# Performance work log

Measured on AMD Instinct MI355X. Metric: run time of the kernel, lower is better.

The kernel has to match this reference:

```python
import jax, jax.numpy as jnp
import numpy as np
from jax import lax

B, S, H, NH, FF, L, V = 4, 512, 768, 12, 3072, 6, 30522
DH = H // NH


def layer_norm(x, g, b, eps=1e-12):
    mu = x.mean(-1, keepdims=True)
    var = ((x - mu) ** 2).mean(-1, keepdims=True)
    return (x - mu) * lax.rsqrt(var + eps) * g + b


def crf_log_likelihood(emissions, tags, mask, start_t, end_t, trans):
    # torchcrf math, batch_first: emissions [B,S,T], tags [B,S], mask [B,S] bool
    Bn = emissions.shape[0]
    maskf = mask.astype(emissions.dtype)
    barange = jnp.arange(Bn)
    # gold-path (numerator) score
    first = tags[:, 0]
    num = start_t[first] + emissions[barange, 0, first]
    prev, cur = tags[:, :-1], tags[:, 1:]
    trans_sc = trans[prev, cur]                                   # [B,S-1]
    em_sc = jnp.take_along_axis(emissions[:, 1:], cur[..., None], axis=2)[..., 0]
    num = num + jnp.sum((trans_sc + em_sc) * maskf[:, 1:], axis=1)
    last_idx = jnp.sum(mask, axis=1).astype(jnp.int32) - 1
    num = num + end_t[tags[barange, last_idx]]
    # partition function via forward-algorithm scan over time
    alpha0 = start_t[None, :] + emissions[:, 0]                   # [B,T]
    def step(alpha, xs):
        em_t, m_t = xs
        nxt = jax.nn.logsumexp(alpha[:, :, None] + trans[None] + em_t[:, None, :], axis=1)
        return jnp.where(m_t[:, None], nxt, alpha), None
    xs = (jnp.swapaxes(emissions[:, 1:], 0, 1), jnp.swapaxes(mask[:, 1:], 0, 1))
    alpha, _ = lax.scan(step, alpha0, xs)
    logZ = jax.nn.logsumexp(alpha + end_t[None, :], axis=1)
    return num - logZ


def bert_qa_emissions(input_ids, attention_mask, token_type_ids, word_emb, pos_emb, type_emb,
                      emb_ln_g, emb_ln_b, Wq, bq, Wk, bk, Wv, bv, Wo, bo, ln1_g, ln1_b,
                      W1, b1, W2, b2, ln2_g, ln2_b, qa_w, qa_b):
    x = word_emb[input_ids] + pos_emb[None, :S] + type_emb[token_type_ids]
    x = layer_norm(x, emb_ln_g, emb_ln_b)
    bias = (1.0 - attention_mask.astype(jnp.float32))[:, None, None, :] * -1e9
    scale = 1.0 / float(np.sqrt(DH))
    for l in range(L):
        q = (x @ Wq[l] + bq[l]).reshape(B, S, NH, DH)
        k = (x @ Wk[l] + bk[l]).reshape(B, S, NH, DH)
        v = (x @ Wv[l] + bv[l]).reshape(B, S, NH, DH)
        att = jnp.einsum('bqhd,bkhd->bhqk', q, k) * scale + bias
        p = jax.nn.softmax(att, axis=-1)
        o = jnp.einsum('bhqk,bkhd->bqhd', p, v).reshape(B, S, H)
        x = layer_norm(x + o @ Wo[l] + bo[l], ln1_g[l], ln1_b[l])
        h = jax.nn.gelu(x @ W1[l] + b1[l], approximate=False)
        x = layer_norm(x + h @ W2[l] + b2[l], ln2_g[l], ln2_b[l])
    # qa_outputs: start_logits = col 0, end_logits = col 1 == stack([start,end], dim=2)
    return x @ qa_w + qa_b                                        # [B,S,2]


def setup_inputs() -> dict:
    key = jax.random.key(0)
    ks = jax.random.split(key, 20)
    g = lambda k, shape: jax.random.normal(k, shape, jnp.float32) * 0.02
    u = lambda k, shape: jax.random.uniform(k, shape, jnp.float32, -0.1, 0.1)
    return {
        'input_ids': jax.random.randint(ks[0], (B, S), 0, V),
        'attention_mask': jnp.ones((B, S), jnp.int32),
        'token_type_ids': jnp.zeros((B, S), jnp.int32),
        'start_positions': jax.random.randint(ks[1], (B,), 0, 200),
        'end_positions': jax.random.randint(ks[2], (B,), 0, 400),
        'word_emb': g(ks[3], (V, H)),
        'pos_emb': g(ks[4], (S, H)),
        'type_emb': g(ks[5], (2, H)),
        'emb_ln_g': jnp.ones((H,), jnp.float32), 'emb_ln_b': jnp.zeros((H,), jnp.float32),
        'Wq': g(ks[6], (L, H, H)), 'bq': jnp.zeros((L, H), jnp.float32),
        'Wk': g(ks[7], (L, H, H)), 'bk': jnp.zeros((L, H), jnp.float32),
        'Wv': g(ks[8], (L, H, H)), 'bv': jnp.zeros((L, H), jnp.float32),
        'Wo': g(ks[9], (L, H, H)), 'bo': jnp.zeros((L, H), jnp.float32),
        'ln1_g': jnp.ones((L, H), jnp.float32), 'ln1_b': jnp.zeros((L, H), jnp.float32),
        'W1': g(ks[10], (L, H, FF)), 'b1': jnp.zeros((L, FF), jnp.float32),
        'W2': g(ks[11], (L, FF, H)), 'b2': jnp.zeros((L, H), jnp.float32),
        'ln2_g': jnp.ones((L, H), jnp.float32), 'ln2_b': jnp.zeros((L, H), jnp.float32),
        'qa_w': g(ks[12], (H, 2)), 'qa_b': jnp.zeros((2,), jnp.float32),
        'crf_start': u(ks[13], (2,)), 'crf_end': u(ks[14], (2,)), 'crf_trans': u(ks[15], (2, 2)),
    }


def reference(input_ids, attention_mask, token_type_ids, start_positions, end_positions,
              word_emb, pos_emb, type_emb, emb_ln_g, emb_ln_b, Wq, bq, Wk, bk, Wv, bv,
              Wo, bo, ln1_g, ln1_b, W1, b1, W2, b2, ln2_g, ln2_b, qa_w, qa_b,
              crf_start, crf_end, crf_trans):
    emissions = bert_qa_emissions(input_ids, attention_mask, token_type_ids, word_emb, pos_emb,
                                  type_emb, emb_ln_g, emb_ln_b, Wq, bq, Wk, bk, Wv, bv, Wo, bo,
                                  ln1_g, ln1_b, W1, b1, W2, b2, ln2_g, ln2_b, qa_w, qa_b)
    # labels[i, start:end+1] = 1 when 0 <= start <= end < S, else all zeros (matches torch loop)
    pos = jnp.arange(S)
    sp = start_positions[:, None]
    ep = end_positions[:, None]
    valid = (sp >= 0) & (sp < S) & (ep >= 0) & (ep < S) & (sp <= ep)
    labels = jnp.where(valid & (pos >= sp) & (pos <= ep), 1, 0)
    mask = attention_mask.astype(bool)
    llh = crf_log_likelihood(emissions, labels, mask, crf_start, crf_end, crf_trans)
    return -jnp.sum(llh)  # torchcrf reduction='sum'; loss = -crf(...)
```

## Files before the change

### kernel.cpp

```cpp
#include <hip/hip_runtime.h>
#include <hip/hip_bf16.h>
#include <math.h>

#define B_  4
#define S_  512
#define H_  768
#define NH_ 12
#define DH_ 64
#define FF_ 3072
#define L_  6
#define V_  30522
#define QKVN 2304
#define M_  (B_ * S_)

typedef short s16x8 __attribute__((ext_vector_type(8)));
typedef short s16x4v __attribute__((ext_vector_type(4)));
typedef float f32x4 __attribute__((ext_vector_type(4)));

__device__ __forceinline__ void gload_lds16(const void* g, void* l) {
    __builtin_amdgcn_global_load_lds(
        (const __attribute__((address_space(1))) void*)g,
        (__attribute__((address_space(3))) void*)l,
        16, 0, 0);
}

__device__ __forceinline__ ushort f2bu(float x) {
    __hip_bfloat16 h = __float2bfloat16(x);
    return *(ushort*)&h;
}

__device__ __forceinline__ s16x8 lds_frag(const ushort* p) {
    s16x4v lo = *(const s16x4v*)p;
    s16x4v hi = *(const s16x4v*)(p + 4);
    return __builtin_shufflevector(lo, hi, 0, 1, 2, 3, 4, 5, 6, 7);
}

__device__ __forceinline__ s16x8 lds_frag16(const ushort* p) {
    return *(const s16x8*)p;
}

__device__ __forceinline__ void embed_body(
    const int* __restrict__ ids, const int* __restrict__ tt,
    const float* __restrict__ wemb, const float* __restrict__ pemb,
    const float* __restrict__ temb, const float* __restrict__ g,
    const float* __restrict__ bb, float* __restrict__ x,
    __hip_bfloat16* __restrict__ xb, float* red)
{
    const int t = blockIdx.x;
    const int s = t % S_;
    const int tid = threadIdx.x;

    const float* wr = wemb + (size_t)ids[t] * H_;
    const float* pr = pemb + (size_t)s * H_;
    const float* tr = temb + (size_t)tt[t] * H_;

    float v[3];
    float sum = 0.f;
#pragma unroll
    for (int i = 0; i < 3; i++) {
        int c = tid + i * 256;
        v[i] = wr[c] + pr[c] + tr[c];
        sum += v[i];
    }
    red[tid] = sum; __syncthreads();
    for (int st = 128; st > 0; st >>= 1) { if (tid < st) red[tid] += red[tid + st]; __syncthreads(); }
    const float mean = red[0] / (float)H_;
    __syncthreads();
    float s2 = 0.f;
#pragma unroll
    for (int i = 0; i < 3; i++) { float d = v[i] - mean; s2 += d * d; }
    red[tid] = s2; __syncthreads();
    for (int st = 128; st > 0; st >>= 1) { if (tid < st) red[tid] += red[tid + st]; __syncthreads(); }
    const float rstd = rsqrtf(red[0] / (float)H_ + 1e-12f);
#pragma unroll
    for (int i = 0; i < 3; i++) {
        int c = tid + i * 256;
        float o = (v[i] - mean) * rstd * g[c] + bb[c];
        x[(size_t)t * H_ + c] = o;
        xb[(size_t)t * H_ + c] = __float2bfloat16(o);
    }
}

__global__ __launch_bounds__(256) void prep_embed_kernel(
    const float* __restrict__ Wq, const float* __restrict__ Wk,
    const float* __restrict__ Wv, const float* __restrict__ Wo,
    const float* __restrict__ W1, const float* __restrict__ W2,
    const float* __restrict__ bq, const float* __restrict__ bk,
    const float* __restrict__ bv,
    ushort* __restrict__ Wt_qkv, ushort* __restrict__ Wt_o,
    ushort* __restrict__ Wt_1, ushort* __restrict__ Wt_2,
    float* __restrict__ b_qkv,
    const int* __restrict__ ids, const int* __restrict__ tt,
    const float* __restrict__ wemb, const float* __restrict__ pemb,
    const float* __restrict__ temb, const float* __restrict__ eg,
    const float* __restrict__ eb, float* __restrict__ x,
    __hip_bfloat16* __restrict__ xb)
{
    __shared__ float tile[64][68];

    if (blockIdx.y == L_) {
        embed_body(ids, tt, wemb, pemb, temb, eg, eb, x, xb, (float*)tile);
        return;
    }

    const int l  = blockIdx.y;
    const int id = blockIdx.x;
    if (id >= 1737) return;
    const int tid = threadIdx.x;

    if (id >= 1728) {
        int i = (id - 1728) * 256 + tid;
        if (i < QKVN)
            b_qkv[(size_t)l * QKVN + i] =
                (i < H_) ? bq[l * H_ + i]
                         : ((i < 2 * H_) ? bk[l * H_ + i - H_] : bv[l * H_ + i - 2 * H_]);
        return;
    }

    const float* src; ushort* dst; int N, ncols, ktiles, t;
    if (id < 432) {
        const int mat = id / 144; t = id % 144;
        src = (mat == 0) ? (Wq + (size_t)l * H_ * H_)
            : (mat == 1) ? (Wk + (size_t)l * H_ * H_)
                         : (Wv + (size_t)l * H_ * H_);
        dst = Wt_qkv + (size_t)l * 3 * H_ * H_ + (size_t)mat * H_ * H_;
        N = H_; ncols = 12; ktiles = 12;
    } else if (id < 576) {
        t = id - 432;
        src = Wo + (size_t)l * H_ * H_;
        dst = Wt_o + (size_t)l * H_ * H_;
        N = H_; ncols = 12; ktiles = 12;
    } else if (id < 1152) {
        t = id - 576;
        src = W1 + (size_t)l * H_ * FF_;
        dst = Wt_1 + (size_t)l * H_ * FF_;
        N = FF_; ncols = 48; ktiles = 12;
    } else {
        t = id - 1152;
        src = W2 + (size_t)l * FF_ * H_;
        dst = Wt_2 + (size_t)l * FF_ * H_;
        N = H_; ncols = 12; ktiles = 48;
    }

    const int n0 = (t % ncols) * 64;
    const int k0 = (t / ncols) * 64;

    const int lr = tid >> 4;
    const int lc = tid & 15;
#pragma unroll
    for (int i = 0; i < 4; i++)
        *(f32x4*)&tile[lr + 16 * i][lc * 4] =
            *(const f32x4*)&src[(size_t)(k0 + lr + 16 * i) * N + n0 + lc * 4];
    __syncthreads();

    const int rn = tid >> 2;
    const int kc = tid & 3;
    s16x8 o0, o1;
#pragma unroll
    for (int j = 0; j < 8; j++) o0[j] = (short)f2bu(tile[kc * 16 + j][rn]);
#pragma unroll
    for (int j = 0; j < 8; j++) o1[j] = (short)f2bu(tile[kc * 16 + 8 + j][rn]);
    ushort* dp = dst + ((size_t)(n0 >> 6) * ktiles + (k0 >> 6)) * 4096 + tid * 16;
    *(s16x8*)dp       = o0;
    *(s16x8*)(dp + 8) = o1;
}

#define TM 128
#define TN 128
#define TK 64

template<int EPI, int OUTBF, int NS>
__global__ __launch_bounds__(256) void gemm_mfma_kernel(
    const ushort* __restrict__ A, const ushort* __restrict__ Bt,
    const float* __restrict__ bias, void* __restrict__ Cout,
    int M, int K, int N)
{
    __shared__ alignas(16) ushort As[2][TM * TK];
    __shared__ alignas(16) ushort Bs[2][TN * TK];
    const int tid  = threadIdx.x;
    const int lane = tid & 63;
    const int wave = tid >> 6;
    const int m0 = blockIdx.y * TM;
    const int n0 = blockIdx.x * TN;
    const int wm = (wave >> 1) * 64;
    const int wn = (wave & 1) * 64;

    const int Ksub = K / NS;
    const int Kt   = K >> 6;
    int kt0 = 0;
    if (NS > 1) {
        A  += (size_t)blockIdx.z * Ksub;
        kt0 = blockIdx.z * (Ksub >> 6);
    }

    f32x4 acc[4][4];
#pragma unroll
    for (int i = 0; i < 4; i++)
#pragma unroll
        for (int j = 0; j < 4; j++)
            acc[i][j] = (f32x4){0.f, 0.f, 0.f, 0.f};

    const int r8 = lane >> 3;
    const int sl = lane & 7;
    const int gk = (sl ^ r8) * 8;
    const ushort* aSrc[4];
    const ushort* bSrc[4];
    int dOff[4];
#pragma unroll
    for (int c = 0; c < 4; c++) {
        const int R = wave * 32 + c * 8;
        aSrc[c] = A + (size_t)(m0 + R + r8) * K + gk;
        const int n = n0 + R + r8;
        bSrc[c] = Bt + ((size_t)(n >> 6) * Kt + kt0) * 4096 + (n & 63) * 64 + gk;
        dOff[c] = R * TK;
    }

    const int fr = lane & 15;
    const int q4 = lane >> 4;
    int offA[4][2], offB[4][2];
#pragma unroll
    for (int i = 0; i < 4; i++) {
        const int rowA = wm + i * 16 + fr;
        const int rowB = wn + i * 16 + fr;
#pragma unroll
        for (int ks = 0; ks < 2; ks++) {
            offA[i][ks] = rowA * TK + (((ks * 4 + q4) ^ (rowA & 7)) * 8);
            offB[i][ks] = rowB * TK + (((ks * 4 + q4) ^ (rowB & 7)) * 8);
        }
    }

    const int niter = Ksub / TK;

#pragma unroll
    for (int c = 0; c < 4; c++) {
        gload_lds16(aSrc[c], &As[0][dOff[c]]);
        gload_lds16(bSrc[c], &Bs[0][dOff[c]]);
    }

    int cur = 0;
    for (int it = 0; it < niter; ++it) {
        __syncthreads();
        if (it + 1 < niter) {
            const int koff = (it + 1) * TK;
            const size_t boff = (size_t)(it + 1) * 4096;
#pragma unroll
            for (int c = 0; c < 4; c++) {
                gload_lds16(aSrc[c] + koff, &As[cur ^ 1][dOff[c]]);
                gload_lds16(bSrc[c] + boff, &Bs[cur ^ 1][dOff[c]]);
            }
        }

#pragma unroll
        for (int ks = 0; ks < 2; ks++) {
            s16x8 af[4], bf[4];
#pragma unroll
            for (int i = 0; i < 4; i++) af[i] = lds_frag16(&As[cur][offA[i][ks]]);
#pragma unroll
            for (int j = 0; j < 4; j++) bf[j] = lds_frag16(&Bs[cur][offB[j][ks]]);
#pragma unroll
            for (int i = 0; i < 4; i++)
#pragma unroll
                for (int j = 0; j < 4; j++)
                    acc[i][j] = __builtin_amdgcn_mfma_f32_16x16x32_bf16(
                        af[i], bf[j], acc[i][j], 0, 0, 0);
        }
        cur ^= 1;
    }

    const int ecol = lane & 15;
    const int erow = (lane >> 4) * 4;
    float* outF = (float*)Cout + (size_t)blockIdx.z * M * N;
#pragma unroll
    for (int j = 0; j < 4; j++) {
        const int gcol = n0 + wn + j * 16 + ecol;
        const float bv = (NS == 1 || blockIdx.z == 0) ? bias[gcol] : 0.f;
#pragma unroll
        for (int i = 0; i < 4; i++) {
#pragma unroll
            for (int r = 0; r < 4; r++) {
                const int grow = m0 + wm + i * 16 + erow + r;
                float v = acc[i][j][r] + bv;
                if (EPI == 1) v = v * 0.5f * (1.0f + erff(v * 0.70710678118654752f));
                if (OUTBF)
                    ((ushort*)Cout)[(size_t)grow * N + gcol] = f2bu(v);
                else
                    outF[(size_t)grow * N + gcol] = v;
            }
        }
    }
}

#define VST 68

__global__ __launch_bounds__(256) void flash_attn_mfma_kernel(
    const ushort* __restrict__ QKV, const int* __restrict__ amask,
    __hip_bfloat16* __restrict__ Octx)
{
    const int q0 = blockIdx.x * 64, h = blockIdx.y, b = blockIdx.z;
    const int tid = threadIdx.x, lane = tid & 63, wave = tid >> 6;
    __shared__ ushort Qs[64 * VST];
    __shared__ ushort Ks[64 * VST];
    __shared__ ushort Vt[64 * VST];
    __shared__ ushort Ps[4][16 * VST];
    __shared__ float biasS[S_];

    for (int i = tid; i < S_; i += 256)
        biasS[i] = amask[b * S_ + i] ? 0.f : -1e9f;

    {
        const ushort* qb = QKV + (size_t)(b * S_ + q0) * QKVN + h * DH_;
        const int q = tid >> 2, dg = (tid & 3) * 16;
        s16x8 v0 = *(const s16x8*)(qb + (size_t)q * QKVN + dg);
        s16x8 v1 = *(const s16x8*)(qb + (size_t)q * QKVN + dg + 8);
        ushort* d = &Qs[q * VST + dg];
        *(s16x4v*)(d)      = __builtin_shufflevector(v0, v0, 0, 1, 2, 3);
        *(s16x4v*)(d + 4)  = __builtin_shufflevector(v0, v0, 4, 5, 6, 7);
        *(s16x4v*)(d + 8)  = __builtin_shufflevector(v1, v1, 0, 1, 2, 3);
        *(s16x4v*)(d + 12) = __builtin_shufflevector(v1, v1, 4, 5, 6, 7);
    }
    __syncthreads();

    const int fm = lane & 15;
    const int fk = (lane >> 4) * 8;

    const s16x8 aq0 = lds_frag(&Qs[(wave * 16 + fm) * VST + fk]);
    const s16x8 aq1 = lds_frag(&Qs[(wave * 16 + fm) * VST + 32 + fk]);

    f32x4 acc[4];
#pragma unroll
    for (int j = 0; j < 4; j++) acc[j] = (f32x4){0.f, 0.f, 0.f, 0.f};
    float m_i[4], l_i[4];
#pragma unroll
    for (int r = 0; r < 4; r++) { m_i[r] = -INFINITY; l_i[r] = 0.f; }

    for (int kt = 0; kt < S_; kt += 64) {
        __syncthreads();
        {
            const ushort* kb = QKV + (size_t)(b * S_ + kt) * QKVN + H_ + h * DH_;
            const int ky = tid >> 2, dg = (tid & 3) * 16;
            s16x8 v0 = *(const s16x8*)(kb + (size_t)ky * QKVN + dg);
            s16x8 v1 = *(const s16x8*)(kb + (size_t)ky * QKVN + dg + 8);
            ushort* d = &Ks[ky * VST + dg];
            *(s16x4v*)(d)      = __builtin_shufflevector(v0, v0, 0, 1, 2, 3);
            *(s16x4v*)(d + 4)  = __builtin_shufflevector(v0, v0, 4, 5, 6, 7);
            *(s16x4v*)(d + 8)  = __builtin_shufflevector(v1, v1, 0, 1, 2, 3);
            *(s16x4v*)(d + 12) = __builtin_shufflevector(v1, v1, 4, 5, 6, 7);
        }
        {
            const ushort* vb = QKV + (size_t)(b * S_ + kt) * QKVN + 2 * H_ + h * DH_;
            const int d = tid & 63, kg = tid >> 6;
#pragma unroll
            for (int kp = 0; kp < 8; kp++) {
                const int key = kg * 16 + kp * 2;
                ushort u0 = vb[(size_t)key * QKVN + d];
                ushort u1 = vb[(size_t)(key + 1) * QKVN + d];
                ushort2 u; u.x = u0; u.y = u1;
                *(ushort2*)&Vt[d * VST + key] = u;
            }
        }
        __syncthreads();

        f32x4 sc[4];
#pragma unroll
        for (int jj = 0; jj < 4; jj++) {
            s16x8 b0 = lds_frag(&Ks[(jj * 16 + fm) * VST + fk]);
            s16x8 b1 = lds_frag(&Ks[(jj * 16 + fm) * VST + 32 + fk]);
            f32x4 z = (f32x4){0.f, 0.f, 0.f, 0.f};
            z = __builtin_amdgcn_mfma_f32_16x16x32_bf16(aq0, b0, z, 0, 0, 0);
            z = __builtin_amdgcn_mfma_f32_16x16x32_bf16(aq1, b1, z, 0, 0, 0);
            sc[jj] = z;
        }

#pragma unroll
        for (int r = 0; r < 4; r++) {
            float mx = -INFINITY;
#pragma unroll
            for (int jj = 0; jj < 4; jj++) {
                float v = sc[jj][r] * 0.125f + biasS[kt + jj * 16 + fm];
                sc[jj][r] = v;
                mx = fmaxf(mx, v);
            }
#pragma unroll
            for (int msk = 1; msk < 16; msk <<= 1) mx = fmaxf(mx, __shfl_xor(mx, msk));
            const float newm = fmaxf(m_i[r], mx);
            const float alpha = __expf(m_i[r] - newm);
            m_i[r] = newm;
            float rs = 0.f;
#pragma unroll
            for (int jj = 0; jj < 4; jj++) {
                float p = __expf(sc[jj][r] - newm);
                sc[jj][r] = p; rs += p;
            }
#pragma unroll
            for (int msk = 1; msk < 16; msk <<= 1) rs += __shfl_xor(rs, msk);
            l_i[r] = l_i[r] * alpha + rs;
#pragma unroll
            for (int jj = 0; jj < 4; jj++) acc[jj][r] *= alpha;
        }

#pragma unroll
        for (int jj = 0; jj < 4; jj++)
#pragma unroll
            for (int r = 0; r < 4; r++)
                Ps[wave][((lane >> 4) * 4 + r) * VST + jj * 16 + fm] = f2bu(sc[jj][r]);

        const s16x8 ap0 = lds_frag(&Ps[wave][fm * VST + fk]);
        const s16x8 ap1 = lds_frag(&Ps[wave][fm * VST + 32 + fk]);

#pragma unroll
        for (int jj = 0; jj < 4; jj++) {
            s16x8 b0 = lds_frag(&Vt[(jj * 16 + fm) * VST + fk]);
            s16x8 b1 = lds_frag(&Vt[(jj * 16 + fm) * VST + 32 + fk]);
            acc[jj] = __builtin_amdgcn_mfma_f32_16x16x32_bf16(ap0, b0, acc[jj], 0, 0, 0);
            acc[jj] = __builtin_amdgcn_mfma_f32_16x16x32_bf16(ap1, b1, acc[jj], 0, 0, 0);
        }
    }

#pragma unroll
    for (int r = 0; r < 4; r++) {
        const int q = q0 + wave * 16 + (lane >> 4) * 4 + r;
        const float inv = 1.0f / l_i[r];
        __hip_bfloat16* op = Octx + (size_t)(b * S_ + q) * H_ + h * DH_;
#pragma unroll
        for (int jj = 0; jj < 4; jj++)
            op[jj * 16 + fm] = __float2bfloat16(acc[jj][r] * inv);
    }
}

template<int NS, int QA>
__global__ __launch_bounds__(256) void add_ln_kernel(
    float* __restrict__ x, const float* __restrict__ delta,
    const float* __restrict__ g, const float* __restrict__ bb,
    __hip_bfloat16* __restrict__ xb,
    const float* __restrict__ qa_w, const float* __restrict__ qa_b,
    float* __restrict__ em)
{
    const int t = blockIdx.x;
    const int tid = threadIdx.x;
    __shared__ float red[256];
    __shared__ float red2[256];
    const size_t base = (size_t)t * H_;

    float v[3];
    float sum = 0.f;
#pragma unroll
    for (int i = 0; i < 3; i++) {
        int c = tid + i * 256;
        float d = x[base + c];
#pragma unroll
        for (int s = 0; s < NS; s++)
            d += delta[(size_t)s * M_ * H_ + base + c];
        v[i] = d;
        sum += d;
    }
    red[tid] = sum; __syncthreads();
    for (int st = 128; st > 0; st >>= 1) { if (tid < st) red[tid] += red[tid + st]; __syncthreads(); }
    const float mean = red[0] / (float)H_;
    __syncthreads();
    float s2 = 0.f;
#pragma unroll
    for (int i = 0; i < 3; i++) { float d = v[i] - mean; s2 += d * d; }
    red[tid] = s2; __syncthreads();
    for (int st = 128; st > 0; st >>= 1) { if (tid < st) red[tid] += red[tid + st]; __syncthreads(); }
    const float rstd = rsqrtf(red[0] / (float)H_ + 1e-12f);
    float s0 = 0.f, s1 = 0.f;
#pragma unroll
    for (int i = 0; i < 3; i++) {
        int c = tid + i * 256;
        float o = (v[i] - mean) * rstd * g[c] + bb[c];
        x[base + c] = o;
        xb[base + c] = __float2bfloat16(o);
        if (QA) {
            s0 += o * qa_w[c * 2 + 0];
            s1 += o * qa_w[c * 2 + 1];
        }
    }
    if (QA) {
        __syncthreads();
        red[tid] = s0; red2[tid] = s1; __syncthreads();
        for (int st = 128; st > 0; st >>= 1) {
            if (tid < st) { red[tid] += red[tid + st]; red2[tid] += red2[tid + st]; }
            __syncthreads();
        }
        if (tid == 0) {
            em[(size_t)t * 2 + 0] = red[0] + qa_b[0];
            em[(size_t)t * 2 + 1] = red2[0] + qa_b[1];
        }
    }
}

__device__ __forceinline__ float lse2(float a, float b) {
    float m = fmaxf(a, b);
    return m + log1pf(expf(-fabsf(a - b)));
}

__device__ __forceinline__ float4 lsem_comb(float4 a, float4 b) {
    float4 r;
    r.x = lse2(a.x + b.x, a.y + b.z);
    r.y = lse2(a.x + b.y, a.y + b.w);
    r.z = lse2(a.z + b.x, a.w + b.z);
    r.w = lse2(a.z + b.y, a.w + b.w);
    return r;
}

__global__ __launch_bounds__(256) void crf_parallel_kernel(
    const float* __restrict__ em, const int* __restrict__ amask,
    const int* __restrict__ spos, const int* __restrict__ epos,
    const float* __restrict__ startT, const float* __restrict__ endT,
    const float* __restrict__ trans, float* __restrict__ out)
{
    __shared__ float4 mats[B_][64];
    __shared__ float numred[B_][64];
    __shared__ float cntred[B_][64];
    __shared__ float llh[B_];
    const int tid = threadIdx.x;
    const int s = tid >> 6;
    const int j = tid & 63;
    const float NEG = -1e30f;

    const int sp = spos[s], ep = epos[s];
    const bool valid = (sp >= 0) && (sp < S_) && (ep >= 0) && (ep < S_) && (sp <= ep);
    const float* e = em + (size_t)s * S_ * 2;
    const int* mk = amask + s * S_;
    const float t00 = trans[0], t01 = trans[1], t10 = trans[2], t11 = trans[3];

    float4 C = make_float4(0.f, NEG, NEG, 0.f);
    float num = 0.f, cnt = 0.f;
#pragma unroll
    for (int k = 0; k < 8; k++) {
        const int t = j * 8 + 1 + k;
        float4 Mt = make_float4(0.f, NEG, NEG, 0.f);
        if (t < S_ && mk[t]) {
            const float e0 = e[2 * t], e1 = e[2 * t + 1];
            Mt = make_float4(t00 + e0, t01 + e1, t10 + e0, t11 + e1);
            const int tp = (valid && (t - 1) >= sp && (t - 1) <= ep) ? 1 : 0;
            const int tc = (valid && t >= sp && t <= ep) ? 1 : 0;
            const float tr = tp ? (tc ? t11 : t10) : (tc ? t01 : t00);
            num += tr + (tc ? e1 : e0);
            cnt += 1.f;
        }
        C = (k == 0) ? Mt : lsem_comb(C, Mt);
    }
    if (j == 0) {
        const int tag0 = (valid && 0 >= sp && 0 <= ep) ? 1 : 0;
        num += startT[tag0] + e[tag0];
        cnt += mk[0] ? 1.f : 0.f;
    }
    mats[s][j] = C;
    numred[s][j] = num;
    cntred[s][j] = cnt;
    __syncthreads();

    for (int st = 32; st >= 1; st >>= 1) {
        float4 a, b;
        const bool act = (j < st);
        if (act) { a = mats[s][2 * j]; b = mats[s][2 * j + 1]; }
        __syncthreads();
        if (act) mats[s][j] = lsem_comb(a, b);
        __syncthreads();
    }
    for (int st = 32; st >= 1; st >>= 1) {
        if (j < st) {
            numred[s][j] += numred[s][j + st];
            cntred[s][j] += cntred[s][j + st];
        }
        __syncthreads();
    }

    if (j == 0) {
        float numT = numred[s][0];
        const int last_idx = (int)(cntred[s][0] + 0.5f) - 1;
        const int ltag = (valid && last_idx >= sp && last_idx <= ep) ? 1 : 0;
        numT += endT[ltag];
        const float a00 = startT[0] + e[0];
        const float a01 = startT[1] + e[1];
        const float4 P = mats[s][0];
        const float aF0 = lse2(a00 + P.x, a01 + P.z);
        const float aF1 = lse2(a00 + P.y, a01 + P.w);
        const float logZ = lse2(aF0 + endT[0], aF1 + endT[1]);
        llh[s] = numT - logZ;
    }
    __syncthreads();
    if (tid == 0)
        out[0] = -(llh[0] + llh[1] + llh[2] + llh[3]);
}

extern "C" void kernel_launch(void* const* d_in, const int* in_sizes, int n_in,
                              void* d_out, int out_size, void* d_ws, size_t ws_size,
                              hipStream_t stream)
{
    const int*   input_ids  = (const int*)  d_in[0];
    const int*   attn_mask  = (const int*)  d_in[1];
    const int*   token_type = (const int*)  d_in[2];
    const int*   start_pos  = (const int*)  d_in[3];
    const int*   end_pos    = (const int*)  d_in[4];
    const float* word_emb   = (const float*)d_in[5];
    const float* pos_emb    = (const float*)d_in[6];
    const float* type_emb   = (const float*)d_in[7];
    const float* emb_ln_g   = (const float*)d_in[8];
    const float* emb_ln_b   = (const float*)d_in[9];
    const float* Wq         = (const float*)d_in[10];
    const float* bq         = (const float*)d_in[11];
    const float* Wk         = (const float*)d_in[12];
    const float* bk         = (const float*)d_in[13];
    const float* Wv         = (const float*)d_in[14];
    const float* bv         = (const float*)d_in[15];
    const float* Wo         = (const float*)d_in[16];
    const float* bo         = (const float*)d_in[17];
    const float* ln1_g      = (const float*)d_in[18];
    const float* ln1_b      = (const float*)d_in[19];
    const float* W1         = (const float*)d_in[20];
    const float* b1         = (const float*)d_in[21];
    const float* W2         = (const float*)d_in[22];
    const float* b2         = (const float*)d_in[23];
    const float* ln2_g      = (const float*)d_in[24];
    const float* ln2_b      = (const float*)d_in[25];
    const float* qa_w       = (const float*)d_in[26];
    const float* qa_b       = (const float*)d_in[27];
    const float* crf_start  = (const float*)d_in[28];
    const float* crf_end    = (const float*)d_in[29];
    const float* crf_trans  = (const float*)d_in[30];
    float* out = (float*)d_out;

    float*  x      = (float*)d_ws;
    float*  tmp768 = x + (size_t)M_ * H_;
    float*  emis   = tmp768 + (size_t)4 * M_ * H_;
    float*  b_qkv  = emis + (size_t)M_ * 2;
    ushort* xb     = (ushort*)(b_qkv + (size_t)L_ * QKVN);
    ushort* qkvb   = xb + (size_t)M_ * H_;
    ushort* ctxb   = qkvb + (size_t)M_ * QKVN;
    ushort* hb     = ctxb + (size_t)M_ * H_;
    ushort* Wt_qkv = hb + (size_t)M_ * FF_;
    ushort* Wt_o   = Wt_qkv + (size_t)L_ * QKVN * H_;
    ushort* Wt_1   = Wt_o + (size_t)L_ * H_ * H_;
    ushort* Wt_2   = Wt_1 + (size_t)L_ * H_ * FF_;

    dim3 blk(256);

    prep_embed_kernel<<<dim3(2048, L_ + 1), blk, 0, stream>>>(
        Wq, Wk, Wv, Wo, W1, W2, bq, bk, bv,
        Wt_qkv, Wt_o, Wt_1, Wt_2, b_qkv,
        input_ids, token_type, word_emb, pos_emb, type_emb,
        emb_ln_g, emb_ln_b, x, (__hip_bfloat16*)xb);

    const dim3 gQKV(QKVN / TN, M_ / TM);
    const dim3 gO(H_ / TN, M_ / TM, 2);
    const dim3 gF1(FF_ / TN, M_ / TM);
    const dim3 gF2(H_ / TN, M_ / TM, 4);
    const dim3 gA(S_ / 64, NH_, B_);

    for (int l = 0; l < L_; l++) {
        gemm_mfma_kernel<0, 1, 1><<<gQKV, blk, 0, stream>>>(
            xb, Wt_qkv + (size_t)l * QKVN * H_, b_qkv + (size_t)l * QKVN,
            qkvb, M_, H_, QKVN);

        flash_attn_mfma_kernel<<<gA, blk, 0, stream>>>(
            qkvb, attn_mask, (__hip_bfloat16*)ctxb);

        gemm_mfma_kernel<0, 0, 2><<<gO, blk, 0, stream>>>(
            ctxb, Wt_o + (size_t)l * H_ * H_, bo + l * H_, tmp768, M_, H_, H_);
        add_ln_kernel<2, 0><<<M_, blk, 0, stream>>>(
            x, tmp768, ln1_g + l * H_, ln1_b + l * H_,
            (__hip_bfloat16*)xb, nullptr, nullptr, nullptr);

        gemm_mfma_kernel<1, 1, 1><<<gF1, blk, 0, stream>>>(
            xb, Wt_1 + (size_t)l * H_ * FF_, b1 + l * FF_, hb, M_, H_, FF_);
        gemm_mfma_kernel<0, 0, 4><<<gF2, blk, 0, stream>>>(
            hb, Wt_2 + (size_t)l * FF_ * H_, b2 + l * H_, tmp768, M_, FF_, H_);
        if (l == L_ - 1)
            add_ln_kernel<4, 1><<<M_, blk, 0, stream>>>(
                x, tmp768, ln2_g + l * H_, ln2_b + l * H_,
                (__hip_bfloat16*)xb, qa_w, qa_b, emis);
        else
            add_ln_kernel<4, 0><<<M_, blk, 0, stream>>>(
                x, tmp768, ln2_g + l * H_, ln2_b + l * H_,
                (__hip_bfloat16*)xb, nullptr, nullptr, nullptr);
    }

    crf_parallel_kernel<<<1, 256, 0, stream>>>(emis, attn_mask, start_pos, end_pos,
                                               crf_start, crf_end, crf_trans, out);
}
```

Before: 1.013 ms.

## Overlap next-layer weight conversion with current layer's QKV, attention and FFN1 kernels

The upfront prep kernel now converts only layer 0 weights, alongside the embedding. Conversion of layer l+1's QKV, Wo/W1 and W2 tiles is spread across extra blocks appended to the QKV GEMM, attention and FFN1 launches of layer l. This hides fp32-to-bf16 transpose work in the tails and idle slots of compute kernels, shrinking the large serial prep launch. In exchange it adds grid padding, extra kernel parameters and shared-memory aliasing, and the extra blocks compete for bandwidth with the main work.

```diff
diff --git a/kernel.cpp b/kernel.cpp
--- a/kernel.cpp
+++ b/kernel.cpp
@@ -39,49 +39,8 @@
     return *(const s16x8*)p;
 }
 
-__device__ __forceinline__ void embed_body(
-    const int* __restrict__ ids, const int* __restrict__ tt,
-    const float* __restrict__ wemb, const float* __restrict__ pemb,
-    const float* __restrict__ temb, const float* __restrict__ g,
-    const float* __restrict__ bb, float* __restrict__ x,
-    __hip_bfloat16* __restrict__ xb, float* red)
-{
-    const int t = blockIdx.x;
-    const int s = t % S_;
-    const int tid = threadIdx.x;
-
-    const float* wr = wemb + (size_t)ids[t] * H_;
-    const float* pr = pemb + (size_t)s * H_;
-    const float* tr = temb + (size_t)tt[t] * H_;
-
-    float v[3];
-    float sum = 0.f;
-#pragma unroll
-    for (int i = 0; i < 3; i++) {
-        int c = tid + i * 256;
-        v[i] = wr[c] + pr[c] + tr[c];
-        sum += v[i];
-    }
-    red[tid] = sum; __syncthreads();
-    for (int st = 128; st > 0; st >>= 1) { if (tid < st) red[tid] += red[tid + st]; __syncthreads(); }
-    const float mean = red[0] / (float)H_;
-    __syncthreads();
-    float s2 = 0.f;
-#pragma unroll
-    for (int i = 0; i < 3; i++) { float d = v[i] - mean; s2 += d * d; }
-    red[tid] = s2; __syncthreads();
-    for (int st = 128; st > 0; st >>= 1) { if (tid < st) red[tid] += red[tid + st]; __syncthreads(); }
-    const float rstd = rsqrtf(red[0] / (float)H_ + 1e-12f);
-#pragma unroll
-    for (int i = 0; i < 3; i++) {
-        int c = tid + i * 256;
-        float o = (v[i] - mean) * rstd * g[c] + bb[c];
-        x[(size_t)t * H_ + c] = o;
-        xb[(size_t)t * H_ + c] = __float2bfloat16(o);
-    }
-}
-
-__global__ __launch_bounds__(256) void prep_embed_kernel(
+__device__ __forceinline__ void prep_tile_body(
+    int id, int l,
     const float* __restrict__ Wq, const float* __restrict__ Wk,
     const float* __restrict__ Wv, const float* __restrict__ Wo,
     const float* __restrict__ W1, const float* __restrict__ W2,
@@ -89,23 +48,8 @@
     const float* __restrict__ bv,
     ushort* __restrict__ Wt_qkv, ushort* __restrict__ Wt_o,
     ushort* __restrict__ Wt_1, ushort* __restrict__ Wt_2,
-    float* __restrict__ b_qkv,
-    const int* __restrict__ ids, const int* __restrict__ tt,
-    const float* __restrict__ wemb, const float* __restrict__ pemb,
-    const float* __restrict__ temb, const float* __restrict__ eg,
-    const float* __restrict__ eb, float* __restrict__ x,
-    __hip_bfloat16* __restrict__ xb)
-{
-    __shared__ float tile[64][68];
-
-    if (blockIdx.y == L_) {
-        embed_body(ids, tt, wemb, pemb, temb, eg, eb, x, xb, (float*)tile);
-        return;
-    }
-
-    const int l  = blockIdx.y;
-    const int id = blockIdx.x;
-    if (id >= 1737) return;
+    float* __restrict__ b_qkv, float (*tile)[68])
+{
     const int tid = threadIdx.x;
 
     if (id >= 1728) {
@@ -165,6 +109,98 @@
     *(s16x8*)(dp + 8) = o1;
 }
 
+__device__ __forceinline__ void prep_aux(
+    int mode, int t, int l,
+    const float* Wq, const float* Wk, const float* Wv, const float* Wo,
+    const float* W1, const float* W2,
+    const float* bq, const float* bk, const float* bv,
+    ushort* Wt_qkv, ushort* Wt_o, ushort* Wt_1, ushort* Wt_2,
+    float* b_qkv, float (*tile)[68])
+{
+    int canon;
+    if (mode == 0) {
+        if (t >= 441) return;
+        canon = (t < 432) ? t : 1728 + (t - 432);
+    } else if (mode == 1) {
+        if (t >= 720) return;
+        canon = 432 + t;
+    } else {
+        if (t >= 576) return;
+        canon = 1152 + t;
+    }
+    prep_tile_body(canon, l, Wq, Wk, Wv, Wo, W1, W2, bq, bk, bv,
+                   Wt_qkv, Wt_o, Wt_1, Wt_2, b_qkv, tile);
+}
+
+__device__ __forceinline__ void embed_body(
+    const int* __restrict__ ids, const int* __restrict__ tt,
+    const float* __restrict__ wemb, const float* __restrict__ pemb,
+    const float* __restrict__ temb, const float* __restrict__ g,
+    const float* __restrict__ bb, float* __restrict__ x,
+    __hip_bfloat16* __restrict__ xb, float* red)
+{
+    const int t = blockIdx.x;
+    const int s = t % S_;
+    const int tid = threadIdx.x;
+
+    const float* wr = wemb + (size_t)ids[t] * H_;
+    const float* pr = pemb + (size_t)s * H_;
+    const float* tr = temb + (size_t)tt[t] * H_;
+
+    float v[3];
+    float sum = 0.f;
+#pragma unroll
+    for (int i = 0; i < 3; i++) {
+        int c = tid + i * 256;
+        v[i] = wr[c] + pr[c] + tr[c];
+        sum += v[i];
+    }
+    red[tid] = sum; __syncthreads();
+    for (int st = 128; st > 0; st >>= 1) { if (tid < st) red[tid] += red[tid + st]; __syncthreads(); }
+    const float mean = red[0] / (float)H_;
+    __syncthreads();
+    float s2 = 0.f;
+#pragma unroll
+    for (int i = 0; i < 3; i++) { float d = v[i] - mean; s2 += d * d; }
+    red[tid] = s2; __syncthreads();
+    for (int st = 128; st > 0; st >>= 1) { if (tid < st) red[tid] += red[tid + st]; __syncthreads(); }
+    const float rstd = rsqrtf(red[0] / (float)H_ + 1e-12f);
+#pragma unroll
+    for (int i = 0; i < 3; i++) {
+        int c = tid + i * 256;
+        float o = (v[i] - mean) * rstd * g[c] + bb[c];
+        x[(size_t)t * H_ + c] = o;
+        xb[(size_t)t * H_ + c] = __float2bfloat16(o);
+    }
+}
+
+__global__ __launch_bounds__(256) void prep_embed_kernel(
+    const float* __restrict__ Wq, const float* __restrict__ Wk,
+    const float* __restrict__ Wv, const float* __restrict__ Wo,
+    const float* __restrict__ W1, const float* __restrict__ W2,
+    const float* __restrict__ bq, const float* __restrict__ bk,
+    const float* __restrict__ bv,
+    ushort* __restrict__ Wt_qkv, ushort* __restrict__ Wt_o,
+    ushort* __restrict__ Wt_1, ushort* __restrict__ Wt_2,
+    float* __restrict__ b_qkv,
+    const int* __restrict__ ids, const int* __restrict__ tt,
+    const float* __restrict__ wemb, const float* __restrict__ pemb,
+    const float* __restrict__ temb, const float* __restrict__ eg,
+    const float* __restrict__ eb, float* __restrict__ x,
+    __hip_bfloat16* __restrict__ xb)
+{
+    __shared__ __align__(16) float tile[64][68];
+
+    if (blockIdx.y == 1) {
+        embed_body(ids, tt, wemb, pemb, temb, eg, eb, x, xb, (float*)tile);
+        return;
+    }
+    const int id = blockIdx.x;
+    if (id < 1737)
+        prep_tile_body(id, 0, Wq, Wk, Wv, Wo, W1, W2, bq, bk, bv,
+                       Wt_qkv, Wt_o, Wt_1, Wt_2, b_qkv, tile);
+}
+
 #define TM 128
 #define TN 128
 #define TK 64
@@ -173,10 +209,27 @@
 __global__ __launch_bounds__(256) void gemm_mfma_kernel(
     const ushort* __restrict__ A, const ushort* __restrict__ Bt,
     const float* __restrict__ bias, void* __restrict__ Cout,
-    int M, int K, int N)
+    int M, int K, int N,
+    int auxMode, int lnext,
+    const float* Wq, const float* Wk, const float* Wv, const float* Wo,
+    const float* W1, const float* W2,
+    const float* bq, const float* bk, const float* bv,
+    ushort* Wt_qkv, ushort* Wt_o, ushort* Wt_1, ushort* Wt_2,
+    float* b_qkv)
 {
     __shared__ alignas(16) ushort As[2][TM * TK];
     __shared__ alignas(16) ushort Bs[2][TN * TK];
+
+    const int NX = N / TN;
+    if ((int)blockIdx.x >= NX) {
+        if (auxMode >= 0 && blockIdx.z == 0) {
+            const int t = ((int)blockIdx.x - NX) * gridDim.y + blockIdx.y;
+            prep_aux(auxMode, t, lnext, Wq, Wk, Wv, Wo, W1, W2, bq, bk, bv,
+                     Wt_qkv, Wt_o, Wt_1, Wt_2, b_qkv, (float(*)[68])As);
+        }
+        return;
+    }
+
     const int tid  = threadIdx.x;
     const int lane = tid & 63;
     const int wave = tid >> 6;
@@ -294,15 +347,33 @@
 
 __global__ __launch_bounds__(256) void flash_attn_mfma_kernel(
     const ushort* __restrict__ QKV, const int* __restrict__ amask,
-    __hip_bfloat16* __restrict__ Octx)
-{
+    __hip_bfloat16* __restrict__ Octx,
+    int auxMode, int lnext,
+    const float* Wq, const float* Wk, const float* Wv, const float* Wo,
+    const float* W1, const float* W2,
+    const float* bq, const float* bk, const float* bv,
+    ushort* Wt_qkv, ushort* Wt_o, ushort* Wt_1, ushort* Wt_2,
+    float* b_qkv)
+{
+    __shared__ __align__(16) char smem[36864];
+    ushort* const Qs  = (ushort*)smem;
+    ushort* const Ks  = (ushort*)(smem + 8704);
+    ushort* const Vt  = (ushort*)(smem + 17408);
+    ushort* const Ps  = (ushort*)(smem + 26112);
+    float*  const biasS = (float*)(smem + 34816);
+
+    if ((int)blockIdx.x >= S_ / 64) {
+        if (auxMode >= 0) {
+            const int t = ((int)blockIdx.x - S_ / 64) * 48
+                        + (int)blockIdx.y * 4 + (int)blockIdx.z;
+            prep_aux(auxMode, t, lnext, Wq, Wk, Wv, Wo, W1, W2, bq, bk, bv,
+                     Wt_qkv, Wt_o, Wt_1, Wt_2, b_qkv, (float(*)[68])smem);
+        }
+        return;
+    }
+
     const int q0 = blockIdx.x * 64, h = blockIdx.y, b = blockIdx.z;
     const int tid = threadIdx.x, lane = tid & 63, wave = tid >> 6;
-    __shared__ ushort Qs[64 * VST];
-    __shared__ ushort Ks[64 * VST];
-    __shared__ ushort Vt[64 * VST];
-    __shared__ ushort Ps[4][16 * VST];
-    __shared__ float biasS[S_];
 
     for (int i = tid; i < S_; i += 256)
         biasS[i] = amask[b * S_ + i] ? 0.f : -1e9f;
@@ -398,14 +469,15 @@
             for (int jj = 0; jj < 4; jj++) acc[jj][r] *= alpha;
         }
 
+        ushort* const Pw = Ps + wave * 16 * VST;
 #pragma unroll
         for (int jj = 0; jj < 4; jj++)
 #pragma unroll
             for (int r = 0; r < 4; r++)
-                Ps[wave][((lane >> 4) * 4 + r) * VST + jj * 16 + fm] = f2bu(sc[jj][r]);
-
-        const s16x8 ap0 = lds_frag(&Ps[wave][fm * VST + fk]);
-        const s16x8 ap1 = lds_frag(&Ps[wave][fm * VST + 32 + fk]);
+                Pw[((lane >> 4) * 4 + r) * VST + jj * 16 + fm] = f2bu(sc[jj][r]);
+
+        const s16x8 ap0 = lds_frag(&Pw[fm * VST + fk]);
+        const s16x8 ap1 = lds_frag(&Pw[fm * VST + 32 + fk]);
 
 #pragma unroll
         for (int jj = 0; jj < 4; jj++) {
@@ -637,36 +709,53 @@
 
     dim3 blk(256);
 
-    prep_embed_kernel<<<dim3(2048, L_ + 1), blk, 0, stream>>>(
+    prep_embed_kernel<<<dim3(2048, 2), blk, 0, stream>>>(
         Wq, Wk, Wv, Wo, W1, W2, bq, bk, bv,
         Wt_qkv, Wt_o, Wt_1, Wt_2, b_qkv,
         input_ids, token_type, word_emb, pos_emb, type_emb,
         emb_ln_g, emb_ln_b, x, (__hip_bfloat16*)xb);
 
-    const dim3 gQKV(QKVN / TN, M_ / TM);
-    const dim3 gO(H_ / TN, M_ / TM, 2);
-    const dim3 gF1(FF_ / TN, M_ / TM);
-    const dim3 gF2(H_ / TN, M_ / TM, 4);
-    const dim3 gA(S_ / 64, NH_, B_);
-
     for (int l = 0; l < L_; l++) {
-        gemm_mfma_kernel<0, 1, 1><<<gQKV, blk, 0, stream>>>(
+        const bool host = (l + 1 < L_);
+        const int lnext = l + 1;
+
+        dim3 gQKVl(QKVN / TN + (host ? 28 : 0), M_ / TM);
+        gemm_mfma_kernel<0, 1, 1><<<gQKVl, blk, 0, stream>>>(
             xb, Wt_qkv + (size_t)l * QKVN * H_, b_qkv + (size_t)l * QKVN,
-            qkvb, M_, H_, QKVN);
-
-        flash_attn_mfma_kernel<<<gA, blk, 0, stream>>>(
-            qkvb, attn_mask, (__hip_bfloat16*)ctxb);
-
+            qkvb, M_, H_, QKVN,
+            host ? 0 : -1, lnext,
+            Wq, Wk, Wv, Wo, W1, W2, bq, bk, bv,
+            Wt_qkv, Wt_o, Wt_1, Wt_2, b_qkv);
+
+        dim3 gAl(S_ / 64 + (host ? 15 : 0), NH_, B_);
+        flash_attn_mfma_kernel<<<gAl, blk, 0, stream>>>(
+            qkvb, attn_mask, (__hip_bfloat16*)ctxb,
+            host ? 1 : -1, lnext,
+            Wq, Wk, Wv, Wo, W1, W2, bq, bk, bv,
+            Wt_qkv, Wt_o, Wt_1, Wt_2, b_qkv);
+
+        dim3 gO(H_ / TN, M_ / TM, 2);
         gemm_mfma_kernel<0, 0, 2><<<gO, blk, 0, stream>>>(
-            ctxb, Wt_o + (size_t)l * H_ * H_, bo + l * H_, tmp768, M_, H_, H_);
+            ctxb, Wt_o + (size_t)l * H_ * H_, bo + l * H_, tmp768, M_, H_, H_,
+            -1, 0, Wq, Wk, Wv, Wo, W1, W2, bq, bk, bv,
+            Wt_qkv, Wt_o, Wt_1, Wt_2, b_qkv);
         add_ln_kernel<2, 0><<<M_, blk, 0, stream>>>(
             x, tmp768, ln1_g + l * H_, ln1_b + l * H_,
             (__hip_bfloat16*)xb, nullptr, nullptr, nullptr);
 
-        gemm_mfma_kernel<1, 1, 1><<<gF1, blk, 0, stream>>>(
-            xb, Wt_1 + (size_t)l * H_ * FF_, b1 + l * FF_, hb, M_, H_, FF_);
+        dim3 gF1l(FF_ / TN + (host ? 36 : 0), M_ / TM);
+        gemm_mfma_kernel<1, 1, 1><<<gF1l, blk, 0, stream>>>(
+            xb, Wt_1 + (size_t)l * H_ * FF_, b1 + l * FF_, hb, M_, H_, FF_,
+            host ? 2 : -1, lnext,
+            Wq, Wk, Wv, Wo, W1, W2, bq, bk, bv,
+            Wt_qkv, Wt_o, Wt_1, Wt_2, b_qkv);
+
+        dim3 gF2(H_ / TN, M_ / TM, 4);
         gemm_mfma_kernel<0, 0, 4><<<gF2, blk, 0, stream>>>(
-            hb, Wt_2 + (size_t)l * FF_ * H_, b2 + l * H_, tmp768, M_, FF_, H_);
+            hb, Wt_2 + (size_t)l * FF_ * H_, b2 + l * H_, tmp768, M_, FF_, H_,
+            -1, 0, Wq, Wk, Wv, Wo, W1, W2, bq, bk, bv,
+            Wt_qkv, Wt_o, Wt_1, Wt_2, b_qkv);
+
         if (l == L_ - 1)
             add_ln_kernel<4, 1><<<M_, blk, 0, stream>>>(
                 x, tmp768, ln2_g + l * H_, ln2_b + l * H_,
```

Measured after the change: 1.021 ms. About the same (+0.8%).

## Double-buffer K/V tiles in flash attention with register prefetch

Applied to the files above, without the earlier changes.

The attention kernel now prefetches the next K/V tile into registers while computing on the current one, stores it into a second LDS buffer afterwards, and uses one barrier per iteration instead of two. It also raises wave priority around the MFMA blocks with s_setprio. The embedding/prep kernel is restructured into a helper function with no behavioural change. Extra LDS and registers may lower occupancy.

```diff
diff --git a/kernel.cpp b/kernel.cpp
--- a/kernel.cpp
+++ b/kernel.cpp
@@ -39,49 +39,8 @@
     return *(const s16x8*)p;
 }
 
-__device__ __forceinline__ void embed_body(
-    const int* __restrict__ ids, const int* __restrict__ tt,
-    const float* __restrict__ wemb, const float* __restrict__ pemb,
-    const float* __restrict__ temb, const float* __restrict__ g,
-    const float* __restrict__ bb, float* __restrict__ x,
-    __hip_bfloat16* __restrict__ xb, float* red)
-{
-    const int t = blockIdx.x;
-    const int s = t % S_;
-    const int tid = threadIdx.x;
-
-    const float* wr = wemb + (size_t)ids[t] * H_;
-    const float* pr = pemb + (size_t)s * H_;
-    const float* tr = temb + (size_t)tt[t] * H_;
-
-    float v[3];
-    float sum = 0.f;
-#pragma unroll
-    for (int i = 0; i < 3; i++) {
-        int c = tid + i * 256;
-        v[i] = wr[c] + pr[c] + tr[c];
-        sum += v[i];
-    }
-    red[tid] = sum; __syncthreads();
-    for (int st = 128; st > 0; st >>= 1) { if (tid < st) red[tid] += red[tid + st]; __syncthreads(); }
-    const float mean = red[0] / (float)H_;
-    __syncthreads();
-    float s2 = 0.f;
-#pragma unroll
-    for (int i = 0; i < 3; i++) { float d = v[i] - mean; s2 += d * d; }
-    red[tid] = s2; __syncthreads();
-    for (int st = 128; st > 0; st >>= 1) { if (tid < st) red[tid] += red[tid + st]; __syncthreads(); }
-    const float rstd = rsqrtf(red[0] / (float)H_ + 1e-12f);
-#pragma unroll
-    for (int i = 0; i < 3; i++) {
-        int c = tid + i * 256;
-        float o = (v[i] - mean) * rstd * g[c] + bb[c];
-        x[(size_t)t * H_ + c] = o;
-        xb[(size_t)t * H_ + c] = __float2bfloat16(o);
-    }
-}
-
-__global__ __launch_bounds__(256) void prep_embed_kernel(
+__device__ __forceinline__ void prep_tile_body(
+    int id, int l,
     const float* __restrict__ Wq, const float* __restrict__ Wk,
     const float* __restrict__ Wv, const float* __restrict__ Wo,
     const float* __restrict__ W1, const float* __restrict__ W2,
@@ -89,23 +48,8 @@
     const float* __restrict__ bv,
     ushort* __restrict__ Wt_qkv, ushort* __restrict__ Wt_o,
     ushort* __restrict__ Wt_1, ushort* __restrict__ Wt_2,
-    float* __restrict__ b_qkv,
-    const int* __restrict__ ids, const int* __restrict__ tt,
-    const float* __restrict__ wemb, const float* __restrict__ pemb,
-    const float* __restrict__ temb, const float* __restrict__ eg,
-    const float* __restrict__ eb, float* __restrict__ x,
-    __hip_bfloat16* __restrict__ xb)
+    float* __restrict__ b_qkv, float (*tile)[68])
 {
-    __shared__ float tile[64][68];
-
-    if (blockIdx.y == L_) {
-        embed_body(ids, tt, wemb, pemb, temb, eg, eb, x, xb, (float*)tile);
-        return;
-    }
-
-    const int l  = blockIdx.y;
-    const int id = blockIdx.x;
-    if (id >= 1737) return;
     const int tid = threadIdx.x;
 
     if (id >= 1728) {
@@ -165,6 +109,75 @@
     *(s16x8*)(dp + 8) = o1;
 }
 
+__device__ __forceinline__ void embed_body(
+    const int* __restrict__ ids, const int* __restrict__ tt,
+    const float* __restrict__ wemb, const float* __restrict__ pemb,
+    const float* __restrict__ temb, const float* __restrict__ g,
+    const float* __restrict__ bb, float* __restrict__ x,
+    __hip_bfloat16* __restrict__ xb, float* red)
+{
+    const int t = blockIdx.x;
+    const int s = t % S_;
+    const int tid = threadIdx.x;
+
+    const float* wr = wemb + (size_t)ids[t] * H_;
+    const float* pr = pemb + (size_t)s * H_;
+    const float* tr = temb + (size_t)tt[t] * H_;
+
+    float v[3];
+    float sum = 0.f;
+#pragma unroll
+    for (int i = 0; i < 3; i++) {
+        int c = tid + i * 256;
+        v[i] = wr[c] + pr[c] + tr[c];
+        sum += v[i];
+    }
+    red[tid] = sum; __syncthreads();
+    for (int st = 128; st > 0; st >>= 1) { if (tid < st) red[tid] += red[tid + st]; __syncthreads(); }
+    const float mean = red[0] / (float)H_;
+    __syncthreads();
+    float s2 = 0.f;
+#pragma unroll
+    for (int i = 0; i < 3; i++) { float d = v[i] - mean; s2 += d * d; }
+    red[tid] = s2; __syncthreads();
+    for (int st = 128; st > 0; st >>= 1) { if (tid < st) red[tid] += red[tid + st]; __syncthreads(); }
+    const float rstd = rsqrtf(red[0] / (float)H_ + 1e-12f);
+#pragma unroll
+    for (int i = 0; i < 3; i++) {
+        int c = tid + i * 256;
+        float o = (v[i] - mean) * rstd * g[c] + bb[c];
+        x[(size_t)t * H_ + c] = o;
+        xb[(size_t)t * H_ + c] = __float2bfloat16(o);
+    }
+}
+
+__global__ __launch_bounds__(256) void prep_embed_kernel(
+    const float* __restrict__ Wq, const float* __restrict__ Wk,
+    const float* __restrict__ Wv, const float* __restrict__ Wo,
+    const float* __restrict__ W1, const float* __restrict__ W2,
+    const float* __restrict__ bq, const float* __restrict__ bk,
+    const float* __restrict__ bv,
+    ushort* __restrict__ Wt_qkv, ushort* __restrict__ Wt_o,
+    ushort* __restrict__ Wt_1, ushort* __restrict__ Wt_2,
+    float* __restrict__ b_qkv,
+    const int* __restrict__ ids, const int* __restrict__ tt,
+    const float* __restrict__ wemb, const float* __restrict__ pemb,
+    const float* __restrict__ temb, const float* __restrict__ eg,
+    const float* __restrict__ eb, float* __restrict__ x,
+    __hip_bfloat16* __restrict__ xb)
+{
+    __shared__ __align__(16) float tile[64][68];
+
+    if (blockIdx.y == L_) {
+        embed_body(ids, tt, wemb, pemb, temb, eg, eb, x, xb, (float*)tile);
+        return;
+    }
+    const int id = blockIdx.x;
+    if (id < 1737)
+        prep_tile_body(id, blockIdx.y, Wq, Wk, Wv, Wo, W1, W2, bq, bk, bv,
+                       Wt_qkv, Wt_o, Wt_1, Wt_2, b_qkv, tile);
+}
+
 #define TM 128
 #define TN 128
 #define TK 64
@@ -299,17 +312,52 @@
     const int q0 = blockIdx.x * 64, h = blockIdx.y, b = blockIdx.z;
     const int tid = threadIdx.x, lane = tid & 63, wave = tid >> 6;
     __shared__ ushort Qs[64 * VST];
-    __shared__ ushort Ks[64 * VST];
-    __shared__ ushort Vt[64 * VST];
+    __shared__ ushort Ks[2][64 * VST];
+    __shared__ ushort Vt[2][64 * VST];
     __shared__ ushort Ps[4][16 * VST];
     __shared__ float biasS[S_];
 
     for (int i = tid; i < S_; i += 256)
         biasS[i] = amask[b * S_ + i] ? 0.f : -1e9f;
 
+    const int ky = tid >> 2, dg = (tid & 3) * 16;
+    const int dd = tid & 63, kg = tid >> 6;
+
+    const ushort* kbase = QKV + (size_t)b * S_ * QKVN + H_ + h * DH_;
+    const ushort* vbase = QKV + (size_t)b * S_ * QKVN + 2 * H_ + h * DH_;
+
+    s16x8 kr0, kr1;
+    ushort2 vr[8];
+
+#define LOAD_KV(kt)                                                          \
+    {                                                                        \
+        const ushort* kb = kbase + (size_t)((kt) + ky) * QKVN;               \
+        kr0 = *(const s16x8*)(kb + dg);                                      \
+        kr1 = *(const s16x8*)(kb + dg + 8);                                  \
+        const ushort* vb = vbase + (size_t)(kt) * QKVN + dd;                 \
+        _Pragma("unroll")                                                    \
+        for (int kp = 0; kp < 8; kp++) {                                     \
+            const int key = kg * 16 + kp * 2;                                \
+            vr[kp].x = vb[(size_t)key * QKVN];                               \
+            vr[kp].y = vb[(size_t)(key + 1) * QKVN];                         \
+        }                                                                    \
+    }
+
+#define STORE_KV(buf)                                                        \
+    {                                                                        \
+        ushort* dk = &Ks[buf][ky * VST + dg];                                \
+        *(s16x4v*)(dk)      = __builtin_shufflevector(kr0, kr0, 0, 1, 2, 3); \
+        *(s16x4v*)(dk + 4)  = __builtin_shufflevector(kr0, kr0, 4, 5, 6, 7); \
+        *(s16x4v*)(dk + 8)  = __builtin_shufflevector(kr1, kr1, 0, 1, 2, 3); \
+        *(s16x4v*)(dk + 12) = __builtin_shufflevector(kr1, kr1, 4, 5, 6, 7); \
+        _Pragma("unroll")                                                    \
+        for (int kp = 0; kp < 8; kp++)                                       \
+            *(ushort2*)&Vt[buf][dd * VST + kg * 16 + kp * 2] = vr[kp];       \
+    }
+
     {
         const ushort* qb = QKV + (size_t)(b * S_ + q0) * QKVN + h * DH_;
-        const int q = tid >> 2, dg = (tid & 3) * 16;
+        const int q = tid >> 2;
         s16x8 v0 = *(const s16x8*)(qb + (size_t)q * QKVN + dg);
         s16x8 v1 = *(const s16x8*)(qb + (size_t)q * QKVN + dg + 8);
         ushort* d = &Qs[q * VST + dg];
@@ -318,6 +366,8 @@
         *(s16x4v*)(d + 8)  = __builtin_shufflevector(v1, v1, 0, 1, 2, 3);
         *(s16x4v*)(d + 12) = __builtin_shufflevector(v1, v1, 4, 5, 6, 7);
     }
+    LOAD_KV(0);
+    STORE_KV(0);
     __syncthreads();
 
     const int fm = lane & 15;
@@ -333,43 +383,26 @@
 #pragma unroll
     for (int r = 0; r < 4; r++) { m_i[r] = -INFINITY; l_i[r] = 0.f; }
 
-    for (int kt = 0; kt < S_; kt += 64) {
-        __syncthreads();
-        {
-            const ushort* kb = QKV + (size_t)(b * S_ + kt) * QKVN + H_ + h * DH_;
-            const int ky = tid >> 2, dg = (tid & 3) * 16;
-            s16x8 v0 = *(const s16x8*)(kb + (size_t)ky * QKVN + dg);
-            s16x8 v1 = *(const s16x8*)(kb + (size_t)ky * QKVN + dg + 8);
-            ushort* d = &Ks[ky * VST + dg];
-            *(s16x4v*)(d)      = __builtin_shufflevector(v0, v0, 0, 1, 2, 3);
-            *(s16x4v*)(d + 4)  = __builtin_shufflevector(v0, v0, 4, 5, 6, 7);
-            *(s16x4v*)(d + 8)  = __builtin_shufflevector(v1, v1, 0, 1, 2, 3);
-            *(s16x4v*)(d + 12) = __builtin_shufflevector(v1, v1, 4, 5, 6, 7);
-        }
-        {
-            const ushort* vb = QKV + (size_t)(b * S_ + kt) * QKVN + 2 * H_ + h * DH_;
-            const int d = tid & 63, kg = tid >> 6;
-#pragma unroll
-            for (int kp = 0; kp < 8; kp++) {
-                const int key = kg * 16 + kp * 2;
-                ushort u0 = vb[(size_t)key * QKVN + d];
-                ushort u1 = vb[(size_t)(key + 1) * QKVN + d];
-                ushort2 u; u.x = u0; u.y = u1;
-                *(ushort2*)&Vt[d * VST + key] = u;
-            }
-        }
-        __syncthreads();
+    int cur = 0;
+    for (int ti = 0; ti < S_ / 64; ti++) {
+        const int kt = ti * 64;
+        if (ti + 1 < S_ / 64) LOAD_KV(kt + 64);
+
+        const ushort* Ksc = Ks[cur];
+        const ushort* Vtc = Vt[cur];
 
         f32x4 sc[4];
+        __builtin_amdgcn_s_setprio(1);
 #pragma unroll
         for (int jj = 0; jj < 4; jj++) {
-            s16x8 b0 = lds_frag(&Ks[(jj * 16 + fm) * VST + fk]);
-            s16x8 b1 = lds_frag(&Ks[(jj * 16 + fm) * VST + 32 + fk]);
+            s16x8 b0 = lds_frag(&Ksc[(jj * 16 + fm) * VST + fk]);
+            s16x8 b1 = lds_frag(&Ksc[(jj * 16 + fm) * VST + 32 + fk]);
             f32x4 z = (f32x4){0.f, 0.f, 0.f, 0.f};
             z = __builtin_amdgcn_mfma_f32_16x16x32_bf16(aq0, b0, z, 0, 0, 0);
             z = __builtin_amdgcn_mfma_f32_16x16x32_bf16(aq1, b1, z, 0, 0, 0);
             sc[jj] = z;
         }
+        __builtin_amdgcn_s_setprio(0);
 
 #pragma unroll
         for (int r = 0; r < 4; r++) {
@@ -398,23 +431,34 @@
             for (int jj = 0; jj < 4; jj++) acc[jj][r] *= alpha;
         }
 
+        ushort* const Pw = &Ps[wave][0];
 #pragma unroll
         for (int jj = 0; jj < 4; jj++)
 #pragma unroll
             for (int r = 0; r < 4; r++)
-                Ps[wave][((lane >> 4) * 4 + r) * VST + jj * 16 + fm] = f2bu(sc[jj][r]);
-
-        const s16x8 ap0 = lds_frag(&Ps[wave][fm * VST + fk]);
-        const s16x8 ap1 = lds_frag(&Ps[wave][fm * VST + 32 + fk]);
-
+                Pw[((lane >> 4) * 4 + r) * VST + jj * 16 + fm] = f2bu(sc[jj][r]);
+
+        const s16x8 ap0 = lds_frag(&Pw[fm * VST + fk]);
+        const s16x8 ap1 = lds_frag(&Pw[fm * VST + 32 + fk]);
+
+        __builtin_amdgcn_s_setprio(1);
 #pragma unroll
         for (int jj = 0; jj < 4; jj++) {
-            s16x8 b0 = lds_frag(&Vt[(jj * 16 + fm) * VST + fk]);
-            s16x8 b1 = lds_frag(&Vt[(jj * 16 + fm) * VST + 32 + fk]);
+            s16x8 b0 = lds_frag(&Vtc[(jj * 16 + fm) * VST + fk]);
+            s16x8 b1 = lds_frag(&Vtc[(jj * 16 + fm) * VST + 32 + fk]);
             acc[jj] = __builtin_amdgcn_mfma_f32_16x16x32_bf16(ap0, b0, acc[jj], 0, 0, 0);
             acc[jj] = __builtin_amdgcn_mfma_f32_16x16x32_bf16(ap1, b1, acc[jj], 0, 0, 0);
         }
-    }
+        __builtin_amdgcn_s_setprio(0);
+
+        if (ti + 1 < S_ / 64) {
+            STORE_KV(cur ^ 1);
+            __syncthreads();
+        }
+        cur ^= 1;
+    }
+#undef LOAD_KV
+#undef STORE_KV
 
 #pragma unroll
     for (int r = 0; r < 4; r++) {
```

Result: no change. 1.016 ms (+0.2%).
